# Optimization experiments

Measured on AMD Instinct MI355X. Metric: run time of the kernel, lower is better.

## Reference

```python
import jax, jax.numpy as jnp
import numpy as np

B, T, D = 2048, 200, 64
H1, H2 = 128, 64
NEG_INF = jnp.float32(-(2.0**32) + 1.0)


def setup_inputs() -> dict:
    key = jax.random.key(0)
    ks = jax.random.split(key, 10)
    query = jax.random.normal(ks[0], (B, D), dtype=jnp.float32)
    k = jax.random.normal(ks[1], (B, T, D), dtype=jnp.float32)
    v = jax.random.normal(ks[2], (B, T, D), dtype=jnp.float32)
    mask = jax.random.randint(ks[3], (B, T), 0, 2, dtype=jnp.int32)
    # Deep_layer params: concat width 4*D -> H1 -> H2 -> 1
    s1 = 1.0 / np.sqrt(4 * D)
    s2 = 1.0 / np.sqrt(H1)
    s3 = 1.0 / np.sqrt(H2)
    W1 = jax.random.normal(ks[4], (4 * D, H1), dtype=jnp.float32) * s1
    b1 = jnp.zeros((H1,), dtype=jnp.float32)
    W2 = jax.random.normal(ks[5], (H1, H2), dtype=jnp.float32) * s2
    b2 = jnp.zeros((H2,), dtype=jnp.float32)
    Wo = jax.random.normal(ks[6], (H2, 1), dtype=jnp.float32) * s3
    bo = jnp.zeros((1,), dtype=jnp.float32)
    return {"query": query, "key": k, "value": v, "mask": mask,
            "W1": W1, "b1": b1, "W2": W2, "b2": b2, "Wo": Wo, "bo": bo}


def reference(query, key, value, mask, W1, b1, W2, b2, Wo, bo):
    b, t, d = key.shape
    q = jnp.broadcast_to(query[:, None, :], (b, t, d))          # tile query over T
    emb = jnp.concatenate([q, key, q - key, q * key], axis=-1)  # [B,T,4D]
    h = jax.nn.relu(jnp.einsum('btf,fh->bth', emb, W1) + b1)    # [B,T,H1]
    h = jax.nn.relu(jnp.einsum('bth,hk->btk', h, W2) + b2)      # [B,T,H2]
    score = (jnp.einsum('btk,ko->bto', h, Wo) + bo)[..., 0]     # [B,T]
    score = jnp.where(mask == 0, NEG_INF, score)
    attn = jax.nn.softmax(score, axis=-1)                       # [B,T]
    out = jnp.einsum('bt,btd->bd', attn, value)                 # [B,D]
    return out
```

## Files before the change

### kernel.cpp

```cpp
#include <hip/hip_runtime.h>
#include <hip/hip_bf16.h>
#include <cstdint>
#include <cstddef>

#define NB 2048
#define NT 200
#define ND 64
#define NH1 128
#define NH2 64
#define NTILES 7
#define NTP 224

typedef __bf16 bf16x8 __attribute__((ext_vector_type(8)));
typedef float f32x4 __attribute__((ext_vector_type(4)));

#define MFMA16(A, Bv, C) __builtin_amdgcn_mfma_f32_16x16x32_bf16((A), (Bv), (C), 0, 0, 0)

union BF8u { __bf16 b[8]; bf16x8 v; uint4 u4; };
union BF4u { __bf16 b[4]; uint2 u2; };

template<int N>
__device__ __forceinline__ float row_ror_add(float v) {
    int r = __builtin_amdgcn_update_dpp(0, __builtin_bit_cast(int, v),
                                        0x120 | N, 0xF, 0xF, false);
    return v + __builtin_bit_cast(float, r);
}

__device__ __forceinline__ void bar_sync() {
    __builtin_amdgcn_sched_barrier(0);
    asm volatile("s_waitcnt lgkmcnt(0)" ::: "memory");
    __builtin_amdgcn_s_barrier();
    __builtin_amdgcn_sched_barrier(0);
}

__global__ void prep_kernel(const float* __restrict__ W1, const float* __restrict__ W2,
                            float* __restrict__ Qp, float* __restrict__ AbT,
                            float* __restrict__ PT, __bf16* __restrict__ W2t) {
    int tid = blockIdx.x * blockDim.x + threadIdx.x;
    if (tid < 64 * NH1) {
        int c = tid >> 7, j = tid & 127;
        Qp[tid] = W1[c * NH1 + j] + W1[(128 + c) * NH1 + j];
        int jj = tid >> 6, cc = tid & 63;
        AbT[tid] = W1[(64 + cc) * NH1 + jj] - W1[(128 + cc) * NH1 + jj];
        PT[tid]  = W1[(192 + cc) * NH1 + jj];
        int j2 = tid >> 7, k = tid & 127;
        W2t[tid] = (__bf16)W2[k * NH2 + j2];
    }
}

__global__ __launch_bounds__(256, 4)
void attn_main(const float* __restrict__ query, const float* __restrict__ key,
               const float* __restrict__ value, const int* __restrict__ mask,
               const float* __restrict__ b1, const float* __restrict__ b2,
               const float* __restrict__ Wo,
               const float* __restrict__ Qp, const float* __restrict__ AbT,
               const float* __restrict__ PT, const __bf16* __restrict__ W2t,
               float* __restrict__ out)
{
    __shared__ __align__(16) char smem[22272];
    auto KHI0 = (__bf16(*)[72])(smem);
    auto KHI1 = (__bf16(*)[72])(smem + 4608);
    auto H1   = (__bf16(*)[136])(smem + 9216);
    auto SP   = (float(*)[NTP])(smem + 17920);
    float* QS  = (float*)(smem + 21504);
    float* QHS = (float*)(smem + 21760);
    float* SCORES = (float*)(smem);
    auto REDS = (float(*)[72])(smem + 9216);

    const int b = blockIdx.x;
    const int tid = threadIdx.x;
    const int lane = tid & 63;
    const int wave = tid >> 6;
    const int jn = lane & 15;
    const int g4 = lane >> 4;
    const int g8 = g4 * 8;

    const int r_st = tid >> 3;
    const int c0   = (tid & 7) * 8;
    const float* kp_base = key + (size_t)b * NT * ND + c0;
    float4 pf[2][2];

    {
        const float* kp0 = kp_base + (size_t)r_st * ND;
        pf[0][0] = *(const float4*)(kp0);
        pf[0][1] = *(const float4*)(kp0 + 4);
        const float* kp1 = kp_base + (size_t)(32 + r_st) * ND;
        pf[1][0] = *(const float4*)(kp1);
        pf[1][1] = *(const float4*)(kp1 + 4);
    }

    if (tid < ND) QS[tid] = query[(size_t)b * ND + tid];
    int mk = 0;
    if (tid < NT) mk = mask[(size_t)b * NT + tid];
    bar_sync();

    if (tid < NH1) {
        float a0 = 0.f, a1 = 0.f, a2 = 0.f, a3 = 0.f;
        #pragma unroll
        for (int c = 0; c < ND; c += 4) {
            a0 = fmaf(QS[c],     Qp[c * NH1 + tid],       a0);
            a1 = fmaf(QS[c + 1], Qp[(c + 1) * NH1 + tid], a1);
            a2 = fmaf(QS[c + 2], Qp[(c + 2) * NH1 + tid], a2);
            a3 = fmaf(QS[c + 3], Qp[(c + 3) * NH1 + tid], a3);
        }
        QHS[tid] = b1[tid] + ((a0 + a1) + (a2 + a3));
    }

    bf16x8 g1_b[2][2];
    const int jown = wave * 32;
    #pragma unroll
    for (int n = 0; n < 2; ++n) {
        const int j = jown + n * 16 + jn;
        #pragma unroll
        for (int kk = 0; kk < 2; ++kk) {
            const float* ab = AbT + j * ND + kk * 32 + g8;
            const float* pt = PT  + j * ND + kk * 32 + g8;
            float4 a0 = *(const float4*)ab, a1 = *(const float4*)(ab + 4);
            float4 p0 = *(const float4*)pt, p1 = *(const float4*)(pt + 4);
            const float va[8] = {a0.x,a0.y,a0.z,a0.w,a1.x,a1.y,a1.z,a1.w};
            const float vp[8] = {p0.x,p0.y,p0.z,p0.w,p1.x,p1.y,p1.z,p1.w};
            BF8u vh;
            #pragma unroll
            for (int e = 0; e < 8; ++e) {
                const int c = kk * 32 + g8 + e;
                vh.b[e] = (__bf16)fmaf(QS[c], vp[e], va[e]);
            }
            g1_b[n][kk] = vh.v;
        }
    }
    bf16x8 g2_w[4];
    {
        const int j2 = wave * 16 + jn;
        #pragma unroll
        for (int kk = 0; kk < 4; ++kk)
            g2_w[kk] = *(const bf16x8*)(W2t + j2 * NH1 + kk * 32 + g8);
    }
    bar_sync();

    float qh4[2][4];
    {
        const float4 qa = *(const float4*)(QHS + jown + g4 * 4);
        const float4 qb = *(const float4*)(QHS + jown + 16 + g4 * 4);
        qh4[0][0] = qa.x; qh4[0][1] = qa.y; qh4[0][2] = qa.z; qh4[0][3] = qa.w;
        qh4[1][0] = qb.x; qh4[1][1] = qb.y; qh4[1][2] = qb.z; qh4[1][3] = qb.w;
    }
    const float b2j = b2[wave * 16 + jn];
    const float woj = Wo[wave * 16 + jn];

    #pragma unroll
    for (int ti = 0; ti <= NTILES; ++ti) {
        __bf16 (*KCUR)[72] = (ti & 1) ? KHI1 : KHI0;

        if (ti < NTILES) {
            const int bi = ti & 1;
            const float vals[8] = {pf[bi][0].x, pf[bi][0].y, pf[bi][0].z, pf[bi][0].w,
                                   pf[bi][1].x, pf[bi][1].y, pf[bi][1].z, pf[bi][1].w};
            BF8u ph;
            #pragma unroll
            for (int i = 0; i < 8; ++i) ph.b[i] = (__bf16)vals[i];
            *(uint4*)(&KCUR[r_st][c0]) = ph.u4;
        }
        if (ti > 0) {
            const int t0 = (ti - 1) * 32;
            #pragma unroll
            for (int mt = 0; mt < 2; ++mt) {
                const int arow = mt * 16 + jn;
                const bf16x8 h0v = *(const bf16x8*)(&H1[arow][g8]);
                const bf16x8 h1v = *(const bf16x8*)(&H1[arow][32 + g8]);
                const bf16x8 h2v = *(const bf16x8*)(&H1[arow][64 + g8]);
                const bf16x8 h3v = *(const bf16x8*)(&H1[arow][96 + g8]);
                f32x4 cA = {0.f,0.f,0.f,0.f}, cB = {0.f,0.f,0.f,0.f};
                cA = MFMA16(h0v, g2_w[0], cA);
                cB = MFMA16(h1v, g2_w[1], cB);
                cA = MFMA16(h2v, g2_w[2], cA);
                cB = MFMA16(h3v, g2_w[3], cB);
                #pragma unroll
                for (int r = 0; r < 4; ++r) {
                    float v = fmaxf(cA[r] + cB[r] + b2j, 0.f) * woj;
                    v = row_ror_add<8>(v);
                    v = row_ror_add<4>(v);
                    v = row_ror_add<2>(v);
                    v = row_ror_add<1>(v);
                    if (jn == 0) SP[wave][t0 + mt * 16 + g4 * 4 + r] = v;
                }
            }
        }
        bar_sync();

        if (ti + 2 < NTILES) {
            const int bi = ti & 1;
            int t = (ti + 2) * 32 + r_st;
            t = t < NT ? t : NT - 1;
            const float* kp = kp_base + (size_t)t * ND;
            pf[bi][0] = *(const float4*)(kp);
            pf[bi][1] = *(const float4*)(kp + 4);
        }
        if (ti < NTILES) {
            f32x4 accc[2][2];
            #pragma unroll
            for (int mt = 0; mt < 2; ++mt) {
                const int arow = mt * 16 + jn;
                const bf16x8 k0 = *(const bf16x8*)(&KCUR[arow][g8]);
                const bf16x8 k1 = *(const bf16x8*)(&KCUR[arow][32 + g8]);
                #pragma unroll
                for (int n = 0; n < 2; ++n) {
                    f32x4 ac = {0.f, 0.f, 0.f, 0.f};
                    ac = MFMA16(g1_b[n][0], k0, ac);
                    ac = MFMA16(g1_b[n][1], k1, ac);
                    accc[mt][n] = ac;
                }
            }
            #pragma unroll
            for (int mt = 0; mt < 2; ++mt) {
                const int trow = mt * 16 + jn;
                #pragma unroll
                for (int n = 0; n < 2; ++n) {
                    BF4u pk;
                    #pragma unroll
                    for (int r = 0; r < 4; ++r)
                        pk.b[r] = (__bf16)fmaxf(accc[mt][n][r] + qh4[n][r], 0.f);
                    *(uint2*)(&H1[trow][jown + n * 16 + g4 * 4]) = pk.u2;
                }
            }
            bar_sync();
        }
    }

    const int tg = tid >> 4;
    const int dq = tid & 15;
    const float* vbase = value + (size_t)b * NT * ND + dq * 4;
    const float4 vv0 = *(const float4*)(vbase + (size_t)tg * ND);
    const float4 vv1 = *(const float4*)(vbase + (size_t)(tg + 16) * ND);

    if (tid < NTP) {
        const float sc = SP[0][tid] + SP[1][tid] + SP[2][tid] + SP[3][tid];
        SCORES[tid] = (tid < NT && mk != 0) ? __expf(sc) : 0.f;
    }
    bar_sync();

    {
        const float e0 = SCORES[tg], e1 = SCORES[tg + 16];
        float oa0 = fmaf(e1, vv1.x, e0 * vv0.x);
        float oa1 = fmaf(e1, vv1.y, e0 * vv0.y);
        float oa2 = fmaf(e1, vv1.z, e0 * vv0.z);
        float oa3 = fmaf(e1, vv1.w, e0 * vv0.w);
        float den = e0 + e1;
        #pragma unroll 4
        for (int t = tg + 32; t < NT; t += 16) {
            const float e = SCORES[t];
            const float4 v4 = *(const float4*)(vbase + (size_t)t * ND);
            oa0 = fmaf(e, v4.x, oa0); oa1 = fmaf(e, v4.y, oa1);
            oa2 = fmaf(e, v4.z, oa2); oa3 = fmaf(e, v4.w, oa3);
            den += e;
        }
        REDS[tg][dq*4+0] = oa0; REDS[tg][dq*4+1] = oa1;
        REDS[tg][dq*4+2] = oa2; REDS[tg][dq*4+3] = oa3;
        if (dq == 0) REDS[tg][64] = den;
    }
    bar_sync();

    if (tid < ND) {
        float s = 0.f, den = 0.f;
        #pragma unroll
        for (int g = 0; g < 16; ++g) { s += REDS[g][tid]; den += REDS[g][64]; }
        out[(size_t)b * ND + tid] = s / den;
    }
}

extern "C" void kernel_launch(void* const* d_in, const int* in_sizes, int n_in,
                              void* d_out, int out_size, void* d_ws, size_t ws_size,
                              hipStream_t stream) {
    const float* query = (const float*)d_in[0];
    const float* key   = (const float*)d_in[1];
    const float* value = (const float*)d_in[2];
    const int*   maskp = (const int*)d_in[3];
    const float* W1    = (const float*)d_in[4];
    const float* b1    = (const float*)d_in[5];
    const float* W2    = (const float*)d_in[6];
    const float* b2    = (const float*)d_in[7];
    const float* Wo    = (const float*)d_in[8];
    float* out = (float*)d_out;

    float* Qp  = (float*)d_ws;
    float* AbT = Qp + 64 * NH1;
    float* PT  = AbT + NH1 * ND;
    __bf16* W2t = (__bf16*)(PT + NH1 * ND);

    prep_kernel<<<32, 256, 0, stream>>>(W1, W2, Qp, AbT, PT, W2t);
    attn_main<<<NB, 256, 0, stream>>>(query, key, value, maskp, b1, b2, Wo,
                                      Qp, AbT, PT, W2t, out);
}
```

Baseline: 54.87 us.

## Fuse softmax-weighted value accumulation into the tile loop with prefetched value rows

Moves the exp-and-accumulate-over-value step into the main MLP tile loop. Each tile's scores are consumed one iteration later, and that tile's value rows are loaded one iteration ahead, so the global loads overlap with the MFMA work. This removes the separate scores pass and one block barrier, and precomputes the mask as floats in shared memory. The launch bound is relaxed from 4 to 2 blocks per CU, giving the compiler more registers at the cost of possibly lower occupancy.

```diff
diff --git a/kernel.cpp b/kernel.cpp
--- a/kernel.cpp
+++ b/kernel.cpp
@@ -48,7 +48,7 @@
     }
 }
 
-__global__ __launch_bounds__(256, 4)
+__global__ __launch_bounds__(256, 2)
 void attn_main(const float* __restrict__ query, const float* __restrict__ key,
                const float* __restrict__ value, const int* __restrict__ mask,
                const float* __restrict__ b1, const float* __restrict__ b2,
@@ -57,14 +57,14 @@
                const float* __restrict__ PT, const __bf16* __restrict__ W2t,
                float* __restrict__ out)
 {
-    __shared__ __align__(16) char smem[22272];
+    __shared__ __align__(16) char smem[23168];
     auto KHI0 = (__bf16(*)[72])(smem);
     auto KHI1 = (__bf16(*)[72])(smem + 4608);
     auto H1   = (__bf16(*)[136])(smem + 9216);
     auto SP   = (float(*)[NTP])(smem + 17920);
-    float* QS  = (float*)(smem + 21504);
-    float* QHS = (float*)(smem + 21760);
-    float* SCORES = (float*)(smem);
+    float* MASKF = (float*)(smem + 21504);
+    float* QS  = (float*)(smem + 22400);
+    float* QHS = (float*)(smem + 22656);
     auto REDS = (float(*)[72])(smem + 9216);
 
     const int b = blockIdx.x;
@@ -74,6 +74,8 @@
     const int jn = lane & 15;
     const int g4 = lane >> 4;
     const int g8 = g4 * 8;
+    const int tg = tid >> 4;
+    const int dq = tid & 15;
 
     const int r_st = tid >> 3;
     const int c0   = (tid & 7) * 8;
@@ -90,8 +92,7 @@
     }
 
     if (tid < ND) QS[tid] = query[(size_t)b * ND + tid];
-    int mk = 0;
-    if (tid < NT) mk = mask[(size_t)b * NT + tid];
+    if (tid < NTP) MASKF[tid] = (tid < NT && mask[(size_t)b * NT + tid] != 0) ? 1.f : 0.f;
     bar_sync();
 
     if (tid < NH1) {
@@ -146,6 +147,10 @@
     }
     const float b2j = b2[wave * 16 + jn];
     const float woj = Wo[wave * 16 + jn];
+
+    const float* vbase = value + (size_t)b * NT * ND + dq * 4;
+    float4 vv0{}, vv1{};
+    float oa0 = 0.f, oa1 = 0.f, oa2 = 0.f, oa3 = 0.f, den = 0.f;
 
     #pragma unroll
     for (int ti = 0; ti <= NTILES; ++ti) {
@@ -222,48 +227,50 @@
                     *(uint2*)(&H1[trow][jown + n * 16 + g4 * 4]) = pk.u2;
                 }
             }
-            bar_sync();
-        }
-    }
-
-    const int tg = tid >> 4;
-    const int dq = tid & 15;
-    const float* vbase = value + (size_t)b * NT * ND + dq * 4;
-    const float4 vv0 = *(const float4*)(vbase + (size_t)tg * ND);
-    const float4 vv1 = *(const float4*)(vbase + (size_t)(tg + 16) * ND);
-
-    if (tid < NTP) {
-        const float sc = SP[0][tid] + SP[1][tid] + SP[2][tid] + SP[3][tid];
-        SCORES[tid] = (tid < NT && mk != 0) ? __expf(sc) : 0.f;
-    }
+        }
+        if (ti >= 2) {
+            const int r0 = (ti - 2) * 32 + tg, r1 = r0 + 16;
+            const float s0 = SP[0][r0] + SP[1][r0] + SP[2][r0] + SP[3][r0];
+            const float s1 = SP[0][r1] + SP[1][r1] + SP[2][r1] + SP[3][r1];
+            const float e0 = MASKF[r0] * __expf(s0);
+            const float e1 = MASKF[r1] * __expf(s1);
+            oa0 = fmaf(e0, vv0.x, fmaf(e1, vv1.x, oa0));
+            oa1 = fmaf(e0, vv0.y, fmaf(e1, vv1.y, oa1));
+            oa2 = fmaf(e0, vv0.z, fmaf(e1, vv1.z, oa2));
+            oa3 = fmaf(e0, vv0.w, fmaf(e1, vv1.w, oa3));
+            den += e0 + e1;
+        }
+        if (ti >= 1) {
+            int t0v = (ti - 1) * 32 + tg;      t0v = t0v < NT ? t0v : NT - 1;
+            int t1v = (ti - 1) * 32 + tg + 16; t1v = t1v < NT ? t1v : NT - 1;
+            vv0 = *(const float4*)(vbase + (size_t)t0v * ND);
+            vv1 = *(const float4*)(vbase + (size_t)t1v * ND);
+        }
+        if (ti < NTILES) bar_sync();
+    }
+
+    {
+        const int r0 = (NTILES - 1) * 32 + tg, r1 = r0 + 16;
+        const float s0 = SP[0][r0] + SP[1][r0] + SP[2][r0] + SP[3][r0];
+        const float s1 = SP[0][r1] + SP[1][r1] + SP[2][r1] + SP[3][r1];
+        const float e0 = MASKF[r0] * __expf(s0);
+        const float e1 = MASKF[r1] * __expf(s1);
+        oa0 = fmaf(e0, vv0.x, fmaf(e1, vv1.x, oa0));
+        oa1 = fmaf(e0, vv0.y, fmaf(e1, vv1.y, oa1));
+        oa2 = fmaf(e0, vv0.z, fmaf(e1, vv1.z, oa2));
+        oa3 = fmaf(e0, vv0.w, fmaf(e1, vv1.w, oa3));
+        den += e0 + e1;
+    }
+    REDS[tg][dq*4+0] = oa0; REDS[tg][dq*4+1] = oa1;
+    REDS[tg][dq*4+2] = oa2; REDS[tg][dq*4+3] = oa3;
+    if (dq == 0) REDS[tg][64] = den;
     bar_sync();
 
-    {
-        const float e0 = SCORES[tg], e1 = SCORES[tg + 16];
-        float oa0 = fmaf(e1, vv1.x, e0 * vv0.x);
-        float oa1 = fmaf(e1, vv1.y, e0 * vv0.y);
-        float oa2 = fmaf(e1, vv1.z, e0 * vv0.z);
-        float oa3 = fmaf(e1, vv1.w, e0 * vv0.w);
-        float den = e0 + e1;
-        #pragma unroll 4
-        for (int t = tg + 32; t < NT; t += 16) {
-            const float e = SCORES[t];
-            const float4 v4 = *(const float4*)(vbase + (size_t)t * ND);
-            oa0 = fmaf(e, v4.x, oa0); oa1 = fmaf(e, v4.y, oa1);
-            oa2 = fmaf(e, v4.z, oa2); oa3 = fmaf(e, v4.w, oa3);
-            den += e;
-        }
-        REDS[tg][dq*4+0] = oa0; REDS[tg][dq*4+1] = oa1;
-        REDS[tg][dq*4+2] = oa2; REDS[tg][dq*4+3] = oa3;
-        if (dq == 0) REDS[tg][64] = den;
-    }
-    bar_sync();
-
     if (tid < ND) {
-        float s = 0.f, den = 0.f;
-        #pragma unroll
-        for (int g = 0; g < 16; ++g) { s += REDS[g][tid]; den += REDS[g][64]; }
-        out[(size_t)b * ND + tid] = s / den;
+        float s = 0.f, d = 0.f;
+        #pragma unroll
+        for (int g = 0; g < 16; ++g) { s += REDS[g][tid]; d += REDS[g][64]; }
+        out[(size_t)b * ND + tid] = s / d;
     }
 }
 
```

Result: slower. 56.64 us (+3.2%).
